# Kernel tuning notes

Measured on AMD Instinct MI355X. Metric: run time of the kernel, lower is better.

## Reference

```python
import jax, jax.numpy as jnp
import numpy as np

GRID_SIZE = 5
SPLINE_ORDER = 3

def _grid(in_features, dtype):
    # efficient-KAN default grid over [-1, 1], extended by spline_order knots each side
    h = 2.0 / GRID_SIZE
    g = jnp.arange(-SPLINE_ORDER, GRID_SIZE + SPLINE_ORDER + 1, dtype=dtype) * h - 1.0
    return jnp.broadcast_to(g, (in_features, g.shape[0]))  # (in, G+2k+1)

def _b_splines(x, grid):
    # x: (..., in) -> bases: (..., in, G+k) via Cox-de Boor recursion
    xk = x[..., None]
    bases = ((xk >= grid[:, :-1]) & (xk < grid[:, 1:])).astype(x.dtype)
    for k in range(1, SPLINE_ORDER + 1):
        left = (xk - grid[:, :-(k + 1)]) / (grid[:, k:-1] - grid[:, :-(k + 1)]) * bases[..., :-1]
        right = (grid[:, k + 1:] - xk) / (grid[:, k + 1:] - grid[:, 1:-k]) * bases[..., 1:]
        bases = left + right
    return bases

def _kan_linear(x, base_w, spline_w, scaler):
    # base branch: SiLU(x) @ W_base^T ; spline branch: einsum over B-spline basis
    grid = _grid(base_w.shape[1], x.dtype)
    bases = _b_splines(x, grid)                      # (..., in, G+k)
    scaled = spline_w * scaler[..., None]            # (out, in, G+k)
    base_out = jax.nn.silu(x) @ base_w.T
    spline_out = jnp.einsum('...ig,oig->...o', bases, scaled)
    return base_out + spline_out

def setup_inputs() -> dict:
    key = jax.random.key(0)
    ks = jax.random.split(key, 11)
    B, N, C, O = 2, 256, 64, 64
    GK = GRID_SIZE + SPLINE_ORDER
    return {
        'x': jax.random.normal(ks[0], (B, N, C), jnp.float32),
        'adj': jax.random.randint(ks[1], (B, N, N), 0, 2, jnp.int32),
        'fw_base': jax.random.normal(ks[2], (1, C), jnp.float32) * 0.1,
        'fw_spline': jax.random.normal(ks[3], (1, C, GK), jnp.float32) * 0.1,
        'fw_scaler': jax.random.normal(ks[4], (1, C), jnp.float32) * 0.1,
        'mw_base': jax.random.normal(ks[5], (O, C), jnp.float32) * 0.1,
        'mw_spline': jax.random.normal(ks[6], (O, C, GK), jnp.float32) * 0.1,
        'mw_scaler': jax.random.normal(ks[7], (O, C), jnp.float32) * 0.1,
        'uw_base': jax.random.normal(ks[8], (O, C + O), jnp.float32) * 0.1,
        'uw_spline': jax.random.normal(ks[9], (O, C + O, GK), jnp.float32) * 0.1,
        'uw_scaler': jax.random.normal(ks[10], (O, C + O), jnp.float32) * 0.1,
    }

def reference(x, adj, fw_base, fw_spline, fw_scaler, mw_base, mw_spline, mw_scaler, uw_base, uw_spline, uw_scaler):
    # r_ij = h_i - h_j : (B, N, N, C)
    r_ij = x[:, :, None, :] - x[:, None, :, :]
    energy = _kan_linear(r_ij, fw_base, fw_spline, fw_scaler)[..., 0]  # (B, N, N)
    energy = jnp.where(adj == 0, jnp.asarray(-1e9, energy.dtype), energy)
    alpha = jax.nn.softmax(energy, axis=-1)
    msg_val = _kan_linear(x, mw_base, mw_spline, mw_scaler)            # (B, N, O)
    aggr = jnp.einsum('bij,bjo->bio', alpha, msg_val)
    combined = jnp.concatenate([x, aggr], axis=-1)
    return _kan_linear(combined, uw_base, uw_spline, uw_scaler)
```

## Files before the change

### kernel.cpp

```cpp
#include <hip/hip_runtime.h>
#include <math.h>

#define NB 256
#define CH 64
#define OUTF 64
#define GK 8
#define UIN 128

#define WS_MSG 0
#define WS_CPAD 32768

__device__ __forceinline__ float silu(float v) {
    return v * __builtin_amdgcn_rcpf(1.0f + __expf(-v));
}

__device__ __forceinline__ void spline4(float r, int& d, float4& v) {
    float p = (r + 2.2f) * 2.5f;
    float fd = floorf(p);
    d = (int)fd;
    float u = p - fd;
    if ((unsigned)d > 10u) d = 11;
    float um = 1.0f - u;
    float u2 = u * u, u3 = u2 * u;
    const float k6 = 1.0f / 6.0f;
    v.x = um * um * um * k6;
    v.y = (3.0f * u3 - 6.0f * u2 + 4.0f) * k6;
    v.z = (-3.0f * u3 + 3.0f * u2 + 3.0f * u + 1.0f) * k6;
    v.w = u3 * k6;
}

__device__ __forceinline__ void build_basis(float v, float* row8, float* sil) {
    int d; float4 vv; spline4(v, d, vv);
#pragma unroll
    for (int g = 0; g < 8; ++g) row8[g] = 0.0f;
#pragma unroll
    for (int k = 0; k < 4; ++k) {
        int m = d - 3 + k;
        if ((unsigned)m < 8u) row8[m] = ((const float*)&vv)[k];
    }
    *sil = silu(v);
}

__global__ __launch_bounds__(256, 2) void msg_kernel(
    const float* __restrict__ x,
    const float* __restrict__ fws, const float* __restrict__ fwsc,
    const float* __restrict__ mwb, const float* __restrict__ mws,
    const float* __restrict__ mwsc,
    float* __restrict__ ws) {
    const int blk = blockIdx.x, tid = threadIdx.x;

    if (blk == 512) {
        for (int e = tid; e < CH * 16; e += 256) {
            int c = e >> 4, dd = e & 15;
            float4 cf = make_float4(0.f, 0.f, 0.f, 0.f);
            if (dd <= 10) {
                float sc = fwsc[c];
                float w0 = 0.f, w1 = 0.f, w2 = 0.f, w3 = 0.f;
                int m0 = dd - 3;
                if ((unsigned)(m0 + 0) < 8u) w0 = fws[c * GK + m0 + 0] * sc;
                if ((unsigned)(m0 + 1) < 8u) w1 = fws[c * GK + m0 + 1] * sc;
                if ((unsigned)(m0 + 2) < 8u) w2 = fws[c * GK + m0 + 2] * sc;
                if ((unsigned)(m0 + 3) < 8u) w3 = fws[c * GK + m0 + 3] * sc;
                cf.x = (w0 + 4.0f * w1 + w2) * (1.0f / 6.0f);
                cf.y = (w2 - w0) * 0.5f;
                cf.z = (w0 - 2.0f * w1 + w2) * 0.5f;
                cf.w = (w3 - w0 + 3.0f * (w1 - w2)) * (1.0f / 6.0f);
            }
            ((float4*)(ws + WS_CPAD))[e] = cf;
        }
        return;
    }

    const int row = blk;
    __shared__ __align__(16) float Mb[CH][8];
    __shared__ float Msil[CH];
    __shared__ float part[4][OUTF];

    if (tid < CH)
        build_basis(x[row * CH + tid], Mb[tid], &Msil[tid]);
    __syncthreads();

    const int o = tid & 63, w = tid >> 6;
    const int c0 = w * 16;
    float acc = 0.0f;
#pragma unroll
    for (int cc = 0; cc < 16; cc += 4) {
        float4 sc4 = *(const float4*)&mwsc[o * CH + c0 + cc];
        float4 bw4 = *(const float4*)&mwb[o * CH + c0 + cc];
#pragma unroll
        for (int t = 0; t < 4; ++t) {
            int c = c0 + cc + t;
            const float4* wp = (const float4*)&mws[(o * CH + c) * GK];
            float4 wa = wp[0], wb = wp[1];
            const float* B = Mb[c];
            float s = B[0]*wa.x + B[1]*wa.y + B[2]*wa.z + B[3]*wa.w
                    + B[4]*wb.x + B[5]*wb.y + B[6]*wb.z + B[7]*wb.w;
            acc += s * ((const float*)&sc4)[t] + Msil[c] * ((const float*)&bw4)[t];
        }
    }
    part[w][o] = acc;
    __syncthreads();
    if (tid < OUTF)
        ws[WS_MSG + row * OUTF + tid] =
            part[0][tid] + part[1][tid] + part[2][tid] + part[3][tid];
}

__global__ __launch_bounds__(256, 2) void gat_kernel(
    const float* __restrict__ x, const int* __restrict__ adj,
    const float* __restrict__ fwb,
    const float* __restrict__ uwb, const float* __restrict__ uws,
    const float* __restrict__ uwsc,
    const float* __restrict__ ws,
    float* __restrict__ out) {
    const int b = blockIdx.x >> 8;
    const int i = blockIdx.x & 255;
    const int tid = threadIdx.x;

    __shared__ float4 cpad[CH][16];
    __shared__ float2 xisf[CH];
    __shared__ float alpha[NB];
    __shared__ float comb[UIN];
    __shared__ __align__(16) float Fb[UIN][8];
    __shared__ float Fsil[UIN];
    __shared__ float part[4][OUTF];
    __shared__ float wred[4];

    {
        const float4* cp = (const float4*)(ws + WS_CPAD);
        float4* dst = &cpad[0][0];
#pragma unroll
        for (int e = tid; e < CH * 16; e += 256) dst[e] = cp[e];
    }
    if (tid < CH) {
        float v = x[(b * NB + i) * CH + tid];
        xisf[tid] = make_float2(v, fwb[tid]);
        comb[tid] = v;
    }
    __syncthreads();

    const float4* xjp = (const float4*)(x + (b * NB + tid) * CH);
    float e = 0.0f;
#pragma unroll 4
    for (int q = 0; q < 16; ++q) {
        float4 xv = xjp[q];
#pragma unroll
        for (int t = 0; t < 4; ++t) {
            int c = q * 4 + t;
            float2 xs = xisf[c];
            float r = xs.x - ((const float*)&xv)[t];
            float pp = (r + 2.2f) * 2.5f;
            float fd = floorf(pp);
            int d = (int)fd;
            float u = pp - fd;
            if ((unsigned)d > 10u) d = 11;
            float4 cf = cpad[c][d];
            e += cf.x + u * (cf.y + u * (cf.z + u * cf.w)) + silu(r) * xs.y;
        }
    }
    if (adj[(b * NB + i) * NB + tid] == 0) e = -1e9f;

    float mx = e;
#pragma unroll
    for (int off = 32; off > 0; off >>= 1)
        mx = fmaxf(mx, __shfl_xor(mx, off, 64));
    if ((tid & 63) == 0) wred[tid >> 6] = mx;
    __syncthreads();
    mx = fmaxf(fmaxf(wred[0], wred[1]), fmaxf(wred[2], wred[3]));
    float pexp = __expf(e - mx);
    float sw = pexp;
#pragma unroll
    for (int off = 32; off > 0; off >>= 1)
        sw += __shfl_xor(sw, off, 64);
    __syncthreads();
    if ((tid & 63) == 0) wred[tid >> 6] = sw;
    __syncthreads();
    float denom = wred[0] + wred[1] + wred[2] + wred[3];
    alpha[tid] = pexp * __builtin_amdgcn_rcpf(denom);
    __syncthreads();

    {
        const int o = tid & 63, seg = tid >> 6;
        const float* msgb = ws + WS_MSG + (b * NB + seg * 64) * OUTF;
        float a = 0.0f;
#pragma unroll 8
        for (int jj = 0; jj < 64; ++jj)
            a += alpha[seg * 64 + jj] * msgb[jj * OUTF + o];
        part[seg][o] = a;
    }
    __syncthreads();
    if (tid < OUTF)
        comb[CH + tid] = part[0][tid] + part[1][tid] + part[2][tid] + part[3][tid];
    __syncthreads();

    if (tid < UIN)
        build_basis(comb[tid], Fb[tid], &Fsil[tid]);
    __syncthreads();

    {
        const int o = tid & 63, w = tid >> 6;
        const int c0 = w * 32;
        float acc = 0.0f;
#pragma unroll
        for (int cc = 0; cc < 32; cc += 4) {
            float4 sc4 = *(const float4*)&uwsc[o * UIN + c0 + cc];
            float4 bw4 = *(const float4*)&uwb[o * UIN + c0 + cc];
#pragma unroll
            for (int t = 0; t < 4; ++t) {
                int c = c0 + cc + t;
                const float4* wp = (const float4*)&uws[(o * UIN + c) * GK];
                float4 wa = wp[0], wb = wp[1];
                const float* B = Fb[c];
                float s = B[0]*wa.x + B[1]*wa.y + B[2]*wa.z + B[3]*wa.w
                        + B[4]*wb.x + B[5]*wb.y + B[6]*wb.z + B[7]*wb.w;
                acc += s * ((const float*)&sc4)[t] + Fsil[c] * ((const float*)&bw4)[t];
            }
        }
        part[w][o] = acc;
    }
    __syncthreads();
    if (tid < OUTF)
        out[(b * NB + i) * OUTF + tid] =
            part[0][tid] + part[1][tid] + part[2][tid] + part[3][tid];
}

extern "C" void kernel_launch(void* const* d_in, const int* in_sizes, int n_in,
                              void* d_out, int out_size, void* d_ws, size_t ws_size,
                              hipStream_t stream) {
    const float* x     = (const float*)d_in[0];
    const int*   adj   = (const int*)d_in[1];
    const float* fwb   = (const float*)d_in[2];
    const float* fws   = (const float*)d_in[3];
    const float* fwsc  = (const float*)d_in[4];
    const float* mwb   = (const float*)d_in[5];
    const float* mws   = (const float*)d_in[6];
    const float* mwsc  = (const float*)d_in[7];
    const float* uwb   = (const float*)d_in[8];
    const float* uws   = (const float*)d_in[9];
    const float* uwsc  = (const float*)d_in[10];
    float* out = (float*)d_out;
    float* ws = (float*)d_ws;

    msg_kernel<<<513, 256, 0, stream>>>(x, fws, fwsc, mwb, mws, mwsc, ws);
    gat_kernel<<<512, 256, 0, stream>>>(x, adj, fwb, uwb, uws, uwsc, ws, out);
}
```

Baseline: 122.8 us.

## Transpose x for coalesced energy loads, drop softmax max pass, restructure KAN matvecs

Adds transpose blocks to the prep kernel that write x transposed into workspace, so in the energy loop each thread reads x_j with coalesced column loads instead of strided float4 rows. The softmax max reduction and its extra barriers are removed: masked entries get zero and unmasked get exp(e) directly, with normalization folded into the aggregated vector. This relies on energies staying small enough not to overflow. The KAN matvecs in both kernels are rewritten so lanes map to input features with contiguous weight loads and a wave shuffle reduction per output. Message values are also prefetched into registers.

```diff
diff --git a/kernel.cpp b/kernel.cpp
--- a/kernel.cpp
+++ b/kernel.cpp
@@ -9,6 +9,7 @@
 
 #define WS_MSG 0
 #define WS_CPAD 32768
+#define WS_XT 36864
 
 __device__ __forceinline__ float silu(float v) {
     return v * __builtin_amdgcn_rcpf(1.0f + __expf(-v));
@@ -29,19 +30,20 @@
     v.w = u3 * k6;
 }
 
-__device__ __forceinline__ void build_basis(float v, float* row8, float* sil) {
+template <int W>
+__device__ __forceinline__ void basis_col(float v, float (*Bt)[W], int c) {
     int d; float4 vv; spline4(v, d, vv);
 #pragma unroll
-    for (int g = 0; g < 8; ++g) row8[g] = 0.0f;
+    for (int g = 0; g < 8; ++g) Bt[g][c] = 0.0f;
 #pragma unroll
     for (int k = 0; k < 4; ++k) {
         int m = d - 3 + k;
-        if ((unsigned)m < 8u) row8[m] = ((const float*)&vv)[k];
-    }
-    *sil = silu(v);
-}
-
-__global__ __launch_bounds__(256, 2) void msg_kernel(
+        if ((unsigned)m < 8u) Bt[m][c] = ((const float*)&vv)[k];
+    }
+    Bt[8][c] = silu(v);
+}
+
+__global__ __launch_bounds__(256, 2) void msg_prep_kernel(
     const float* __restrict__ x,
     const float* __restrict__ fws, const float* __restrict__ fwsc,
     const float* __restrict__ mwb, const float* __restrict__ mws,
@@ -49,6 +51,22 @@
     float* __restrict__ ws) {
     const int blk = blockIdx.x, tid = threadIdx.x;
 
+    if (blk >= 513) {
+        __shared__ float tile[64][65];
+        const int blk2 = blk - 513, b = blk2 >> 2, jt = blk2 & 3;
+#pragma unroll
+        for (int it = 0; it < 16; ++it) {
+            int idx = it * 256 + tid, jj = idx >> 6, cc = idx & 63;
+            tile[jj][cc] = x[(b * NB + jt * 64 + jj) * CH + cc];
+        }
+        __syncthreads();
+#pragma unroll
+        for (int it = 0; it < 16; ++it) {
+            int idx = it * 256 + tid, cc = idx >> 6, jj = idx & 63;
+            ws[WS_XT + b * CH * NB + cc * NB + jt * 64 + jj] = tile[jj][cc];
+        }
+        return;
+    }
     if (blk == 512) {
         for (int e = tid; e < CH * 16; e += 256) {
             int c = e >> 4, dd = e & 15;
@@ -71,38 +89,31 @@
         return;
     }
 
-    const int row = blk;
-    __shared__ __align__(16) float Mb[CH][8];
-    __shared__ float Msil[CH];
-    __shared__ float part[4][OUTF];
-
-    if (tid < CH)
-        build_basis(x[row * CH + tid], Mb[tid], &Msil[tid]);
-    __syncthreads();
-
-    const int o = tid & 63, w = tid >> 6;
-    const int c0 = w * 16;
-    float acc = 0.0f;
-#pragma unroll
-    for (int cc = 0; cc < 16; cc += 4) {
-        float4 sc4 = *(const float4*)&mwsc[o * CH + c0 + cc];
-        float4 bw4 = *(const float4*)&mwb[o * CH + c0 + cc];
-#pragma unroll
-        for (int t = 0; t < 4; ++t) {
-            int c = c0 + cc + t;
-            const float4* wp = (const float4*)&mws[(o * CH + c) * GK];
-            float4 wa = wp[0], wb = wp[1];
-            const float* B = Mb[c];
-            float s = B[0]*wa.x + B[1]*wa.y + B[2]*wa.z + B[3]*wa.w
-                    + B[4]*wb.x + B[5]*wb.y + B[6]*wb.z + B[7]*wb.w;
-            acc += s * ((const float*)&sc4)[t] + Msil[c] * ((const float*)&bw4)[t];
-        }
-    }
-    part[w][o] = acc;
-    __syncthreads();
-    if (tid < OUTF)
-        ws[WS_MSG + row * OUTF + tid] =
-            part[0][tid] + part[1][tid] + part[2][tid] + part[3][tid];
+    const int row = blk, lane = tid & 63, w = tid >> 6;
+    __shared__ float Bt[9][CH];
+    if (tid < CH) basis_col<CH>(x[row * CH + tid], Bt, tid);
+    __syncthreads();
+
+    float B[9];
+#pragma unroll
+    for (int g = 0; g < 9; ++g) B[g] = Bt[g][lane];
+
+    float outv = 0.0f;
+#pragma unroll 4
+    for (int oi = 0; oi < 16; ++oi) {
+        int o = w * 16 + oi;
+        const float4* wp = (const float4*)&mws[(o * CH + lane) * GK];
+        float4 wa = wp[0], wb4 = wp[1];
+        float sc = mwsc[o * CH + lane];
+        float bw = mwb[o * CH + lane];
+        float val = (B[0]*wa.x + B[1]*wa.y + B[2]*wa.z + B[3]*wa.w
+                   + B[4]*wb4.x + B[5]*wb4.y + B[6]*wb4.z + B[7]*wb4.w) * sc
+                  + B[8] * bw;
+#pragma unroll
+        for (int off = 32; off > 0; off >>= 1) val += __shfl_xor(val, off, 64);
+        if (lane == oi) outv = val;
+    }
+    if (lane < 16) ws[WS_MSG + row * OUTF + w * 16 + lane] = outv;
 }
 
 __global__ __launch_bounds__(256, 2) void gat_kernel(
@@ -110,117 +121,100 @@
     const float* __restrict__ fwb,
     const float* __restrict__ uwb, const float* __restrict__ uws,
     const float* __restrict__ uwsc,
-    const float* __restrict__ ws,
-    float* __restrict__ out) {
-    const int b = blockIdx.x >> 8;
-    const int i = blockIdx.x & 255;
-    const int tid = threadIdx.x;
+    const float* __restrict__ ws, float* __restrict__ out) {
+    const int b = blockIdx.x >> 8, i = blockIdx.x & 255;
+    const int tid = threadIdx.x, lane = tid & 63, w = tid >> 6;
 
     __shared__ float4 cpad[CH][16];
     __shared__ float2 xisf[CH];
     __shared__ float alpha[NB];
-    __shared__ float comb[UIN];
-    __shared__ __align__(16) float Fb[UIN][8];
-    __shared__ float Fsil[UIN];
+    __shared__ float Bt[9][UIN];
     __shared__ float part[4][OUTF];
     __shared__ float wred[4];
 
     {
         const float4* cp = (const float4*)(ws + WS_CPAD);
         float4* dst = &cpad[0][0];
-#pragma unroll
         for (int e = tid; e < CH * 16; e += 256) dst[e] = cp[e];
     }
     if (tid < CH) {
         float v = x[(b * NB + i) * CH + tid];
         xisf[tid] = make_float2(v, fwb[tid]);
-        comb[tid] = v;
-    }
-    __syncthreads();
-
-    const float4* xjp = (const float4*)(x + (b * NB + tid) * CH);
+        basis_col<UIN>(v, Bt, tid);
+    }
+    __syncthreads();
+
+    float msgv[64];
+    const float* msgb = ws + WS_MSG + (b * NB + w * 64) * OUTF + lane;
+#pragma unroll
+    for (int jj = 0; jj < 64; ++jj) msgv[jj] = msgb[jj * OUTF];
+    const int av = adj[(b * NB + i) * NB + tid];
+
+    const float* xTb = ws + WS_XT + b * CH * NB;
     float e = 0.0f;
+#pragma unroll 8
+    for (int c = 0; c < CH; ++c) {
+        float xj = xTb[c * NB + tid];
+        float2 xs = xisf[c];
+        float r = xs.x - xj;
+        float pp = (r + 2.2f) * 2.5f;
+        float fd = floorf(pp);
+        int d = (int)fd;
+        float u = pp - fd;
+        if ((unsigned)d > 10u) d = 11;
+        float4 cf = cpad[c][d];
+        e += cf.x + u * (cf.y + u * (cf.z + u * cf.w)) + silu(r) * xs.y;
+    }
+    float pexp = av ? __expf(e) : 0.0f;
+    alpha[tid] = pexp;
+    float sw = pexp;
+#pragma unroll
+    for (int off = 32; off > 0; off >>= 1) sw += __shfl_xor(sw, off, 64);
+    if (lane == 0) wred[w] = sw;
+    __syncthreads();
+
+    float rden = __builtin_amdgcn_rcpf(wred[0] + wred[1] + wred[2] + wred[3]);
+
+    {
+        float a = 0.0f;
+#pragma unroll
+        for (int jj = 0; jj < 64; ++jj)
+            a += alpha[w * 64 + jj] * msgv[jj];
+        part[w][lane] = a;
+    }
+    __syncthreads();
+
+    if (tid < OUTF) {
+        float ag = (part[0][tid] + part[1][tid] + part[2][tid] + part[3][tid])
+                 * rden;
+        basis_col<UIN>(ag, Bt, CH + tid);
+    }
+    __syncthreads();
+
+    float BA[9], BB[9];
+#pragma unroll
+    for (int g = 0; g < 9; ++g) {
+        BA[g] = Bt[g][2 * lane];
+        BB[g] = Bt[g][2 * lane + 1];
+    }
+    float outv = 0.0f;
 #pragma unroll 4
-    for (int q = 0; q < 16; ++q) {
-        float4 xv = xjp[q];
-#pragma unroll
-        for (int t = 0; t < 4; ++t) {
-            int c = q * 4 + t;
-            float2 xs = xisf[c];
-            float r = xs.x - ((const float*)&xv)[t];
-            float pp = (r + 2.2f) * 2.5f;
-            float fd = floorf(pp);
-            int d = (int)fd;
-            float u = pp - fd;
-            if ((unsigned)d > 10u) d = 11;
-            float4 cf = cpad[c][d];
-            e += cf.x + u * (cf.y + u * (cf.z + u * cf.w)) + silu(r) * xs.y;
-        }
-    }
-    if (adj[(b * NB + i) * NB + tid] == 0) e = -1e9f;
-
-    float mx = e;
-#pragma unroll
-    for (int off = 32; off > 0; off >>= 1)
-        mx = fmaxf(mx, __shfl_xor(mx, off, 64));
-    if ((tid & 63) == 0) wred[tid >> 6] = mx;
-    __syncthreads();
-    mx = fmaxf(fmaxf(wred[0], wred[1]), fmaxf(wred[2], wred[3]));
-    float pexp = __expf(e - mx);
-    float sw = pexp;
-#pragma unroll
-    for (int off = 32; off > 0; off >>= 1)
-        sw += __shfl_xor(sw, off, 64);
-    __syncthreads();
-    if ((tid & 63) == 0) wred[tid >> 6] = sw;
-    __syncthreads();
-    float denom = wred[0] + wred[1] + wred[2] + wred[3];
-    alpha[tid] = pexp * __builtin_amdgcn_rcpf(denom);
-    __syncthreads();
-
-    {
-        const int o = tid & 63, seg = tid >> 6;
-        const float* msgb = ws + WS_MSG + (b * NB + seg * 64) * OUTF;
-        float a = 0.0f;
-#pragma unroll 8
-        for (int jj = 0; jj < 64; ++jj)
-            a += alpha[seg * 64 + jj] * msgb[jj * OUTF + o];
-        part[seg][o] = a;
-    }
-    __syncthreads();
-    if (tid < OUTF)
-        comb[CH + tid] = part[0][tid] + part[1][tid] + part[2][tid] + part[3][tid];
-    __syncthreads();
-
-    if (tid < UIN)
-        build_basis(comb[tid], Fb[tid], &Fsil[tid]);
-    __syncthreads();
-
-    {
-        const int o = tid & 63, w = tid >> 6;
-        const int c0 = w * 32;
-        float acc = 0.0f;
-#pragma unroll
-        for (int cc = 0; cc < 32; cc += 4) {
-            float4 sc4 = *(const float4*)&uwsc[o * UIN + c0 + cc];
-            float4 bw4 = *(const float4*)&uwb[o * UIN + c0 + cc];
-#pragma unroll
-            for (int t = 0; t < 4; ++t) {
-                int c = c0 + cc + t;
-                const float4* wp = (const float4*)&uws[(o * UIN + c) * GK];
-                float4 wa = wp[0], wb = wp[1];
-                const float* B = Fb[c];
-                float s = B[0]*wa.x + B[1]*wa.y + B[2]*wa.z + B[3]*wa.w
-                        + B[4]*wb.x + B[5]*wb.y + B[6]*wb.z + B[7]*wb.w;
-                acc += s * ((const float*)&sc4)[t] + Fsil[c] * ((const float*)&bw4)[t];
-            }
-        }
-        part[w][o] = acc;
-    }
-    __syncthreads();
-    if (tid < OUTF)
-        out[(b * NB + i) * OUTF + tid] =
-            part[0][tid] + part[1][tid] + part[2][tid] + part[3][tid];
+    for (int oi = 0; oi < 16; ++oi) {
+        int o = w * 16 + oi;
+        const float4* wp = (const float4*)&uws[(o * UIN + 2 * lane) * GK];
+        float4 a0 = wp[0], a1 = wp[1], b0 = wp[2], b1 = wp[3];
+        float2 sc2 = *(const float2*)&uwsc[o * UIN + 2 * lane];
+        float2 bw2 = *(const float2*)&uwb[o * UIN + 2 * lane];
+        float sA = BA[0]*a0.x + BA[1]*a0.y + BA[2]*a0.z + BA[3]*a0.w
+                 + BA[4]*a1.x + BA[5]*a1.y + BA[6]*a1.z + BA[7]*a1.w;
+        float sB = BB[0]*b0.x + BB[1]*b0.y + BB[2]*b0.z + BB[3]*b0.w
+                 + BB[4]*b1.x + BB[5]*b1.y + BB[6]*b1.z + BB[7]*b1.w;
+        float val = sA * sc2.x + BA[8] * bw2.x + sB * sc2.y + BB[8] * bw2.y;
+#pragma unroll
+        for (int off = 32; off > 0; off >>= 1) val += __shfl_xor(val, off, 64);
+        if (lane == oi) outv = val;
+    }
+    if (lane < 16) out[(b * NB + i) * OUTF + w * 16 + lane] = outv;
 }
 
 extern "C" void kernel_launch(void* const* d_in, const int* in_sizes, int n_in,
@@ -240,6 +234,6 @@
     float* out = (float*)d_out;
     float* ws = (float*)d_ws;
 
-    msg_kernel<<<513, 256, 0, stream>>>(x, fws, fwsc, mwb, mws, mwsc, ws);
+    msg_prep_kernel<<<521, 256, 0, stream>>>(x, fws, fwsc, mwb, mws, mwsc, ws);
     gat_kernel<<<512, 256, 0, stream>>>(x, adj, fwb, uwb, uws, uwsc, ws, out);
 }
```

Measured after the change: 120.4 us. No clear change (-1.9%).
